# Kernel optimization log

Hardware: AMD Instinct MI355X
Metric: run time of the kernel (lower is better)

Reference implementation:

```python
import jax, jax.numpy as jnp
import numpy as np

B, S, D, E, R, TOP_K = 4, 4096, 1024, 10, 4, 2
SCALING = 1.0 / R  # alpha / rank


def setup_inputs() -> dict:
    key = jax.random.key(0)
    ks = jax.random.split(key, 7)
    return {
        "x": jax.random.normal(ks[0], (B, S, D), dtype=jnp.float32),
        "W_base": jax.random.normal(ks[1], (D, D), dtype=jnp.float32) * (D ** -0.5),
        "b_base": jax.random.normal(ks[2], (D,), dtype=jnp.float32) * 0.02,
        "gate_W": jax.random.normal(ks[3], (E, D), dtype=jnp.float32) * (D ** -0.5),
        "gate_b": jax.random.normal(ks[4], (E,), dtype=jnp.float32) * 0.02,
        "lora_down": jax.random.normal(ks[5], (E, R, D), dtype=jnp.float32) * (D ** -0.5),
        "lora_up": jax.random.normal(ks[6], (E, D, R), dtype=jnp.float32) * (R ** -0.5),
    }


def reference(x, W_base, b_base, gate_W, gate_b, lora_down, lora_up):
    # Base (frozen) linear: [B,S,D]
    base_out = jnp.einsum("bsd,od->bso", x, W_base) + b_base

    # Top-k gating: logits [B,S,E] -> sparse softmax weights [B,S,E]
    logits = jnp.einsum("bsd,ed->bse", x, gate_W) + gate_b
    top_vals, top_idx = jax.lax.top_k(logits, TOP_K)          # [B,S,K]
    top_w = jax.nn.softmax(top_vals, axis=-1)                 # [B,S,K]
    # scatter top-k weights back to dense [B,S,E] (non-top-k are zero)
    weights = jnp.sum(top_w[..., None] * jax.nn.one_hot(top_idx, E, dtype=x.dtype), axis=-2)

    # All-expert LoRA (matches original loop); weight in rank space to avoid
    # materializing [B,S,E,D]: sum_e w_e * up_e(down_e(x)) * scaling
    h = jnp.einsum("bsd,erd->bser", x, lora_down)             # [B,S,E,R]
    h = h * weights[..., None]
    lora_out = jnp.einsum("bser,edr->bsd", h, lora_up) * SCALING

    return base_out + lora_out
```

## Files before the change

kernel.cpp:

```cpp
#include <hip/hip_runtime.h>
#include <hip/hip_bf16.h>
#include <cstdint>
#include <cstddef>

#define D_DIM 1024
#define E_NUM 10

typedef __attribute__((ext_vector_type(8))) short bf16x8;
typedef __attribute__((ext_vector_type(4))) float f32x4;
typedef unsigned short u16;
typedef unsigned int u32;

__device__ __forceinline__ u16 f2bf(float f) {
  union { float f; u32 u; } v; v.f = f;
  u32 r = v.u + 0x7fffu + ((v.u >> 16) & 1u);
  return (u16)(r >> 16);
}
__device__ __forceinline__ float bf2f(u16 u) {
  union { u32 u; float f; } v; v.u = ((u32)u) << 16; return v.f;
}
__device__ __forceinline__ float dot4(float4 a, float4 b) {
  return a.x * b.x + a.y * b.y + a.z * b.z + a.w * b.w;
}

__global__ void conv_w(const float* __restrict__ W, u16* __restrict__ Wb) {
  const int i = (blockIdx.x * 256 + threadIdx.x) * 8;
  float4 a = *(const float4*)(W + i);
  float4 b = *(const float4*)(W + i + 4);
  *(ushort4*)(Wb + i)     = make_ushort4(f2bf(a.x), f2bf(a.y), f2bf(a.z), f2bf(a.w));
  *(ushort4*)(Wb + i + 4) = make_ushort4(f2bf(b.x), f2bf(b.y), f2bf(b.z), f2bf(b.w));
}

__global__ void prep_ldb(const float* __restrict__ ld, u16* __restrict__ Bld) {
  const int r = blockIdx.x;
  for (int c = threadIdx.x; c < D_DIM; c += 256)
    Bld[r * D_DIM + c] = (r < 40) ? f2bf(ld[r * D_DIM + c]) : (u16)0;
}

__global__ void prep_ub(const float* __restrict__ lup, u16* __restrict__ Ub) {
  const int g = blockIdx.x * 256 + threadIdx.x;
  const int o = g >> 6, j = g & 63;
  Ub[g] = (j < 40) ? f2bf(lup[(size_t)(j >> 2) * (D_DIM * 4) + o * 4 + (j & 3)]) : (u16)0;
}

__global__ __launch_bounds__(256)
void moe_prep_h(const float* __restrict__ x, const u16* __restrict__ Bld,
                u16* __restrict__ hb, u16* __restrict__ xb) {
  __shared__ u16 sX[4][16 * 64];
  __shared__ u16 sB[4][48 * 64];
  __shared__ float sP[4][3][16][17];

  const int tid = threadIdx.x, lane = tid & 63, w = tid >> 6;
  const int r0 = blockIdx.x * 16;
  const int kbase = w * 256;

  f32x4 acc[3] = {};

  float4 av[4];
#pragma unroll
  for (int i = 0; i < 2; ++i) {
    const int c = lane * 2 + i, row = c >> 3, kc = c & 7;
    const float* g = x + (size_t)(r0 + row) * D_DIM + kbase + kc * 8;
    av[i * 2]     = *(const float4*)g;
    av[i * 2 + 1] = *(const float4*)(g + 4);
  }

#pragma unroll 1
  for (int kt = 0; kt < 4; ++kt) {
    const int k0 = kbase + kt * 64;
#pragma unroll
    for (int i = 0; i < 6; ++i) {
      const int c = i * 64 + lane, row = c >> 3, kc = (c & 7) ^ (row & 7);
      __builtin_amdgcn_global_load_lds(
          (const __attribute__((address_space(1))) u32*)(Bld + (size_t)row * D_DIM + k0 + kc * 8),
          (__attribute__((address_space(3))) u32*)&sB[w][c * 8], 16, 0, 0);
    }
#pragma unroll
    for (int i = 0; i < 2; ++i) {
      const int c = lane * 2 + i, row = c >> 3, kc = c & 7;
      const float4 a = av[i * 2], b = av[i * 2 + 1];
      const ushort4 ha = make_ushort4(f2bf(a.x), f2bf(a.y), f2bf(a.z), f2bf(a.w));
      const ushort4 hb4 = make_ushort4(f2bf(b.x), f2bf(b.y), f2bf(b.z), f2bf(b.w));
      const int off = (row * 128 + kc * 16) ^ ((row & 7) << 4);
      *(ushort4*)((char*)sX[w] + off)     = ha;
      *(ushort4*)((char*)sX[w] + off + 8) = hb4;
      if (xb) {
        u16* dst = xb + (size_t)(r0 + row) * D_DIM + k0 + kc * 8;
        *(ushort4*)dst       = ha;
        *(ushort4*)(dst + 4) = hb4;
      }
    }
    __syncthreads();
    if (kt < 3) {
#pragma unroll
      for (int i = 0; i < 2; ++i) {
        const int c = lane * 2 + i, row = c >> 3, kc = c & 7;
        const float* g = x + (size_t)(r0 + row) * D_DIM + (k0 + 64) + kc * 8;
        av[i * 2]     = *(const float4*)g;
        av[i * 2 + 1] = *(const float4*)(g + 4);
      }
    }
#pragma unroll
    for (int kk = 0; kk < 2; ++kk) {
      const int kb = kk * 64 + ((lane >> 4) * 16);
      const int rA = lane & 15;
      const bf16x8 a0 = *(const bf16x8*)((const char*)sX[w] + ((rA * 128 + kb) ^ ((rA & 7) << 4)));
#pragma unroll
      for (int cf = 0; cf < 3; ++cf) {
        const int rB = cf * 16 + (lane & 15);
        const bf16x8 q = *(const bf16x8*)((const char*)sB[w] + ((rB * 128 + kb) ^ ((rB & 7) << 4)));
        acc[cf] = __builtin_amdgcn_mfma_f32_16x16x32_bf16(a0, q, acc[cf], 0, 0, 0);
      }
    }
    __syncthreads();
  }

#pragma unroll
  for (int cf = 0; cf < 3; ++cf)
#pragma unroll
    for (int j = 0; j < 4; ++j)
      sP[w][cf][(lane >> 4) * 4 + j][lane & 15] = acc[cf][j];
  __syncthreads();

  const int row = tid >> 4, c16 = tid & 15;
#pragma unroll
  for (int cf = 0; cf < 3; ++cf) {
    const int col = cf * 16 + c16;
    if (col < 40) {
      const float s = sP[0][cf][row][c16] + sP[1][cf][row][c16] +
                      sP[2][cf][row][c16] + sP[3][cf][row][c16];
      hb[(size_t)(r0 + row) * 40 + col] = f2bf(s);
    }
  }
}

__global__ __launch_bounds__(256)
void moe_gate2(const float* __restrict__ x, const float* __restrict__ gW,
               const float* __restrict__ gb, const u16* __restrict__ hb,
               u16* __restrict__ cd) {
  __shared__ char sXraw[4][16384];
  const int tid = threadIdx.x, lane = tid & 63, w = tid >> 6;
  const int r0 = blockIdx.x * 64;
  const int kq = w * 256;

  float acc[E_NUM] = {};

  float4 pv[16];
#pragma unroll
  for (int i = 0; i < 16; ++i) {
    const int g = i * 64 + lane, tok = g >> 4, f4 = g & 15;
    pv[i] = *(const float4*)(x + (size_t)(r0 + tok) * D_DIM + kq + f4 * 4);
  }

#pragma unroll 1
  for (int c = 0; c < 4; ++c) {
    const int k0 = kq + c * 64;
#pragma unroll
    for (int i = 0; i < 16; ++i) {
      const int g = i * 64 + lane, tok = g >> 4, f4 = g & 15;
      const int off = tok * 256 + ((f4 * 16) ^ ((tok & 7) << 4));
      *(float4*)(sXraw[w] + off) = pv[i];
    }
    float4 xr[16];
#pragma unroll
    for (int k4 = 0; k4 < 16; ++k4) {
      const int off = lane * 256 + ((k4 * 16) ^ ((lane & 7) << 4));
      xr[k4] = *(const float4*)(sXraw[w] + off);
    }
    if (c < 3) {
#pragma unroll
      for (int i = 0; i < 16; ++i) {
        const int g = i * 64 + lane, tok = g >> 4, f4 = g & 15;
        pv[i] = *(const float4*)(x + (size_t)(r0 + tok) * D_DIM + (k0 + 64) + f4 * 4);
      }
    }
#pragma unroll
    for (int e = 0; e < E_NUM; ++e) {
      float s = acc[e];
#pragma unroll
      for (int k4 = 0; k4 < 16; ++k4) {
        const float4 wv = *(const float4*)(gW + e * D_DIM + k0 + k4 * 4);
        s += dot4(xr[k4], wv);
      }
      acc[e] = s;
    }
  }

  {
    float* sp = (float*)sXraw[w];
#pragma unroll
    for (int e = 0; e < E_NUM; ++e) sp[lane * 13 + e] = acc[e];
  }
  __syncthreads();

  if (tid < 64) {
    const int t = r0 + tid;
    float lg[E_NUM];
#pragma unroll
    for (int e = 0; e < E_NUM; ++e) {
      lg[e] = ((const float*)sXraw[0])[tid * 13 + e]
            + ((const float*)sXraw[1])[tid * 13 + e]
            + ((const float*)sXraw[2])[tid * 13 + e]
            + ((const float*)sXraw[3])[tid * 13 + e] + gb[e];
    }
    int e0 = 0; float v0 = lg[0];
#pragma unroll
    for (int e = 1; e < E_NUM; ++e) if (lg[e] > v0) { v0 = lg[e]; e0 = e; }
    int e1 = -1; float v1 = -3.0e38f;
#pragma unroll
    for (int e = 0; e < E_NUM; ++e) if (e != e0 && lg[e] > v1) { v1 = lg[e]; e1 = e; }
    const float pp = expf(v1 - v0);
    const float inv = 1.f / (1.f + pp);
    const float s0 = inv * 0.25f, s1 = pp * inv * 0.25f;

    u16* dst = cd + (size_t)t * 64;
    const u16* hrow = hb + (size_t)t * 40;
#pragma unroll
    for (int e = 0; e < E_NUM; ++e) {
      const float we = (e == e0) ? s0 : ((e == e1) ? s1 : 0.f);
      const ushort4 hh = *(const ushort4*)(hrow + e * 4);
      *(ushort4*)(dst + e * 4) = make_ushort4(
          f2bf(bf2f(hh.x) * we), f2bf(bf2f(hh.y) * we),
          f2bf(bf2f(hh.z) * we), f2bf(bf2f(hh.w) * we));
    }
#pragma unroll
    for (int j = 40; j < 64; j += 4)
      *(ushort4*)(dst + j) = make_ushort4(0, 0, 0, 0);
  }
}

__global__ __launch_bounds__(256, 2)
void moe_gemm_t(const u16* __restrict__ xb, const u16* __restrict__ Wbf,
                const u16* __restrict__ cd, const u16* __restrict__ Ub,
                const float* __restrict__ bias, float* __restrict__ out) {
  __shared__ u16 Al[2][128 * 64];
  __shared__ u16 Bl[2][128 * 64];

  const int tid = threadIdx.x, lane = tid & 63, wid = tid >> 6;
  const int wm = wid >> 1, wn = wid & 1;
  const int p = blockIdx.x;
  const int cx = p & 7, q = p >> 3;
  const int nb = q & 7, mb = cx * 16 + (q >> 3);
  const int m0 = mb * 128, n0 = nb * 128;

  int sc_row[4], sc_kc[4];
#pragma unroll
  for (int i = 0; i < 4; ++i) {
    const int c = i * 256 + tid;
    sc_row[i] = c >> 3;
    sc_kc[i]  = (c & 7) ^ (sc_row[i] & 7);
  }

  f32x4 acc[4][4] = {};

  auto STAGE = [&](int buf, int ktile) {
    const u16* As; const u16* Bs; size_t str; int ko;
    if (ktile < 16) {
      As = xb + (size_t)m0 * D_DIM; Bs = Wbf + (size_t)n0 * D_DIM;
      str = D_DIM; ko = ktile * 64;
    } else {
      As = cd + (size_t)m0 * 64; Bs = Ub + (size_t)n0 * 64;
      str = 64; ko = 0;
    }
#pragma unroll
    for (int i = 0; i < 4; ++i) {
      const int c = i * 256 + tid;
      __builtin_amdgcn_global_load_lds(
          (const __attribute__((address_space(1))) u32*)(As + (size_t)sc_row[i] * str + ko + sc_kc[i] * 8),
          (__attribute__((address_space(3))) u32*)&Al[buf][c * 8], 16, 0, 0);
    }
#pragma unroll
    for (int i = 0; i < 4; ++i) {
      const int c = i * 256 + tid;
      __builtin_amdgcn_global_load_lds(
          (const __attribute__((address_space(1))) u32*)(Bs + (size_t)sc_row[i] * str + ko + sc_kc[i] * 8),
          (__attribute__((address_space(3))) u32*)&Bl[buf][c * 8], 16, 0, 0);
    }
  };

  STAGE(0, 0);
  __syncthreads();

#pragma unroll 1
  for (int kt = 0; kt < 17; ++kt) {
    const int cur = kt & 1;
    if (kt < 16) STAGE(cur ^ 1, kt + 1);
#pragma unroll
    for (int kk = 0; kk < 2; ++kk) {
      bf16x8 af[4], bfr[4];
      const int kb = kk * 64 + ((lane >> 4) * 16);
#pragma unroll
      for (int m = 0; m < 4; ++m) {
        const int row = wm * 64 + m * 16 + (lane & 15);
        af[m] = *(const bf16x8*)((const char*)Al[cur] + ((row * 128 + kb) ^ ((row & 7) << 4)));
      }
#pragma unroll
      for (int n = 0; n < 4; ++n) {
        const int row = wn * 64 + n * 16 + (lane & 15);
        bfr[n] = *(const bf16x8*)((const char*)Bl[cur] + ((row * 128 + kb) ^ ((row & 7) << 4)));
      }
#pragma unroll
      for (int m = 0; m < 4; ++m)
#pragma unroll
        for (int n = 0; n < 4; ++n)
          acc[m][n] = __builtin_amdgcn_mfma_f32_16x16x32_bf16(af[m], bfr[n], acc[m][n], 0, 0, 0);
    }
    __syncthreads();
  }

  const int rg = lane >> 4, cl = lane & 15;
  const int baser = m0 + wm * 64, basec = n0 + wn * 64;
  float bs[4];
#pragma unroll
  for (int n = 0; n < 4; ++n) bs[n] = bias[basec + n * 16 + cl];
#pragma unroll
  for (int m = 0; m < 4; ++m)
#pragma unroll
    for (int j = 0; j < 4; ++j) {
      const int rr = baser + m * 16 + rg * 4 + j;
#pragma unroll
      for (int n = 0; n < 4; ++n)
        out[(size_t)rr * D_DIM + basec + n * 16 + cl] = acc[m][n][j] + bs[n];
    }
}

extern "C" void kernel_launch(void* const* d_in, const int* in_sizes, int n_in,
                              void* d_out, int out_size, void* d_ws, size_t ws_size,
                              hipStream_t stream) {
  const float* x   = (const float*)d_in[0];
  const float* Wb_ = (const float*)d_in[1];
  const float* bb  = (const float*)d_in[2];
  const float* gW  = (const float*)d_in[3];
  const float* gb  = (const float*)d_in[4];
  const float* ld  = (const float*)d_in[5];
  const float* lup = (const float*)d_in[6];

  char* w = (char*)d_ws;
  u16* Wbf = (u16*)w;
  u16* Ub  = (u16*)(w + 2048ull * 1024);
  u16* Bld = (u16*)(w + 2176ull * 1024);
  u16* cd  = (u16*)(w + 2272ull * 1024);
  u16* hb  = (u16*)(w + 4320ull * 1024);
  u16* xb  = (u16*)(w + 5600ull * 1024);

  hipLaunchKernelGGL(conv_w,     dim3(512),  dim3(256), 0, stream, Wb_, Wbf);
  hipLaunchKernelGGL(prep_ldb,   dim3(48),   dim3(256), 0, stream, ld, Bld);
  hipLaunchKernelGGL(prep_ub,    dim3(256),  dim3(256), 0, stream, lup, Ub);
  hipLaunchKernelGGL(moe_prep_h, dim3(1024), dim3(256), 0, stream, x, Bld, hb, xb);
  hipLaunchKernelGGL(moe_gate2,  dim3(256),  dim3(256), 0, stream, x, gW, gb, hb, cd);
  hipLaunchKernelGGL(moe_gemm_t, dim3(1024), dim3(256), 0, stream,
                     xb, Wbf, cd, Ub, bb, (float*)d_out);
}
```

Measured before the change: 123.9 us.

## Shrink gate kernel tile to 16 tokens per block and split K across lanes

After: 119.7 us. 1.04x faster.

```diff
diff --git a/kernel.cpp b/kernel.cpp
--- a/kernel.cpp
+++ b/kernel.cpp
@@ -79,7 +79,7 @@
     for (int i = 0; i < 2; ++i) {
       const int c = lane * 2 + i, row = c >> 3, kc = c & 7;
       const float4 a = av[i * 2], b = av[i * 2 + 1];
-      const ushort4 ha = make_ushort4(f2bf(a.x), f2bf(a.y), f2bf(a.z), f2bf(a.w));
+      const ushort4 ha  = make_ushort4(f2bf(a.x), f2bf(a.y), f2bf(a.z), f2bf(a.w));
       const ushort4 hb4 = make_ushort4(f2bf(b.x), f2bf(b.y), f2bf(b.z), f2bf(b.w));
       const int off = (row * 128 + kc * 16) ^ ((row & 7) << 4);
       *(ushort4*)((char*)sX[w] + off)     = ha;
@@ -135,73 +135,74 @@
 }
 
 __global__ __launch_bounds__(256)
-void moe_gate2(const float* __restrict__ x, const float* __restrict__ gW,
+void moe_gate3(const float* __restrict__ x, const float* __restrict__ gW,
                const float* __restrict__ gb, const u16* __restrict__ hb,
                u16* __restrict__ cd) {
-  __shared__ char sXraw[4][16384];
+  __shared__ char  sRaw[4][4096];
+  __shared__ float sPart[16 * 16 * 11];
+
   const int tid = threadIdx.x, lane = tid & 63, w = tid >> 6;
-  const int r0 = blockIdx.x * 64;
+  const int r0 = blockIdx.x * 16;
   const int kq = w * 256;
+  const int t = lane & 15, s = lane >> 4;
 
   float acc[E_NUM] = {};
 
-  float4 pv[16];
-#pragma unroll
-  for (int i = 0; i < 16; ++i) {
-    const int g = i * 64 + lane, tok = g >> 4, f4 = g & 15;
-    pv[i] = *(const float4*)(x + (size_t)(r0 + tok) * D_DIM + kq + f4 * 4);
+  float4 pv[4];
+#pragma unroll
+  for (int i = 0; i < 4; ++i) {
+    const int f = i * 64 + lane, tok = f >> 4, g = f & 15;
+    pv[i] = *(const float4*)(x + (size_t)(r0 + tok) * D_DIM + kq + g * 4);
   }
 
 #pragma unroll 1
   for (int c = 0; c < 4; ++c) {
     const int k0 = kq + c * 64;
 #pragma unroll
-    for (int i = 0; i < 16; ++i) {
-      const int g = i * 64 + lane, tok = g >> 4, f4 = g & 15;
-      const int off = tok * 256 + ((f4 * 16) ^ ((tok & 7) << 4));
-      *(float4*)(sXraw[w] + off) = pv[i];
-    }
-    float4 xr[16];
-#pragma unroll
-    for (int k4 = 0; k4 < 16; ++k4) {
-      const int off = lane * 256 + ((k4 * 16) ^ ((lane & 7) << 4));
-      xr[k4] = *(const float4*)(sXraw[w] + off);
+    for (int i = 0; i < 4; ++i) {
+      const int f = i * 64 + lane, tok = f >> 4, g = f & 15;
+      *(float4*)(sRaw[w] + tok * 256 + ((g ^ (tok & 15)) << 4)) = pv[i];
+    }
+    float4 xr[4];
+#pragma unroll
+    for (int j = 0; j < 4; ++j) {
+      const int g = s * 4 + j;
+      xr[j] = *(const float4*)(sRaw[w] + t * 256 + ((g ^ (t & 15)) << 4));
     }
     if (c < 3) {
 #pragma unroll
-      for (int i = 0; i < 16; ++i) {
-        const int g = i * 64 + lane, tok = g >> 4, f4 = g & 15;
-        pv[i] = *(const float4*)(x + (size_t)(r0 + tok) * D_DIM + (k0 + 64) + f4 * 4);
-      }
-    }
+      for (int i = 0; i < 4; ++i) {
+        const int f = i * 64 + lane, tok = f >> 4, g = f & 15;
+        pv[i] = *(const float4*)(x + (size_t)(r0 + tok) * D_DIM + (k0 + 64) + g * 4);
+      }
+    }
+    const float* gwk = gW + k0 + s * 16;
 #pragma unroll
     for (int e = 0; e < E_NUM; ++e) {
-      float s = acc[e];
-#pragma unroll
-      for (int k4 = 0; k4 < 16; ++k4) {
-        const float4 wv = *(const float4*)(gW + e * D_DIM + k0 + k4 * 4);
-        s += dot4(xr[k4], wv);
-      }
-      acc[e] = s;
+      float v = acc[e];
+#pragma unroll
+      for (int j = 0; j < 4; ++j)
+        v += dot4(xr[j], *(const float4*)(gwk + e * D_DIM + j * 4));
+      acc[e] = v;
     }
   }
 
   {
-    float* sp = (float*)sXraw[w];
-#pragma unroll
-    for (int e = 0; e < E_NUM; ++e) sp[lane * 13 + e] = acc[e];
+    float* dst = sPart + ((w * 4 + s) * 16 + t) * 11;
+#pragma unroll
+    for (int e = 0; e < E_NUM; ++e) dst[e] = acc[e];
   }
   __syncthreads();
 
-  if (tid < 64) {
-    const int t = r0 + tid;
+  if (tid < 16) {
+    const int tok = tid, tt = r0 + tok;
     float lg[E_NUM];
 #pragma unroll
     for (int e = 0; e < E_NUM; ++e) {
-      lg[e] = ((const float*)sXraw[0])[tid * 13 + e]
-            + ((const float*)sXraw[1])[tid * 13 + e]
-            + ((const float*)sXraw[2])[tid * 13 + e]
-            + ((const float*)sXraw[3])[tid * 13 + e] + gb[e];
+      float v = gb[e];
+#pragma unroll
+      for (int p = 0; p < 16; ++p) v += sPart[(p * 16 + tok) * 11 + e];
+      lg[e] = v;
     }
     int e0 = 0; float v0 = lg[0];
 #pragma unroll
@@ -213,8 +214,8 @@
     const float inv = 1.f / (1.f + pp);
     const float s0 = inv * 0.25f, s1 = pp * inv * 0.25f;
 
-    u16* dst = cd + (size_t)t * 64;
-    const u16* hrow = hb + (size_t)t * 40;
+    u16* dst = cd + (size_t)tt * 64;
+    const u16* hrow = hb + (size_t)tt * 40;
 #pragma unroll
     for (int e = 0; e < E_NUM; ++e) {
       const float we = (e == e0) ? s0 : ((e == e1) ? s1 : 0.f);
@@ -347,7 +348,7 @@
   hipLaunchKernelGGL(prep_ldb,   dim3(48),   dim3(256), 0, stream, ld, Bld);
   hipLaunchKernelGGL(prep_ub,    dim3(256),  dim3(256), 0, stream, lup, Ub);
   hipLaunchKernelGGL(moe_prep_h, dim3(1024), dim3(256), 0, stream, x, Bld, hb, xb);
-  hipLaunchKernelGGL(moe_gate2,  dim3(256),  dim3(256), 0, stream, x, gW, gb, hb, cd);
+  hipLaunchKernelGGL(moe_gate3,  dim3(1024), dim3(256), 0, stream, x, gW, gb, hb, cd);
   hipLaunchKernelGGL(moe_gemm_t, dim3(1024), dim3(256), 0, stream,
                      xb, Wbf, cd, Ub, bb, (float*)d_out);
 }
```
